# Kernel optimization log

Measured on AMD Instinct MI355X. Metric: run time of the kernel, lower is better.

Reference implementation:

```python
import jax, jax.numpy as jnp
import numpy as np

AGENT_RADIUS = 0.5
SAFETY_DIST = 0.1
QP_ITERS = 300


def _qp_solve(p, G, h):
    """Batched QP: min_u 0.5 u^T u + p^T u  s.t.  G u <= h  (Q = I).
    Solved in the dual by projected gradient ascent (differentiable, fixed iters).
    p: [B,2], G: [B,m,2], h: [B,m] -> u: [B,2]
    """
    GGt = jnp.einsum('bmi,bni->bmn', G, G)                 # [B,m,m]
    q = jnp.einsum('bmi,bi->bm', G, p) + h                 # [B,m]
    # Lipschitz upper bound per sample (Frobenius norm of GG^T)
    L = jnp.sqrt(jnp.sum(GGt * GGt, axis=(1, 2))) + 1e-6   # [B]
    alpha = (1.0 / L)[:, None]

    def step(lam, _):
        grad = jnp.einsum('bmn,bn->bm', GGt, lam) + q
        lam = jnp.maximum(lam - alpha * grad, 0.0)
        return lam, None

    lam0 = jnp.zeros_like(h)
    lam, _ = jax.lax.scan(step, lam0, None, length=QP_ITERS)
    u = -p - jnp.einsum('bmi,bm->bi', G, lam)
    return u


def setup_inputs() -> dict:
    key = jax.random.key(0)
    ks = jax.random.split(key, 20)
    B, F, H1, H2 = 8192, 8, 1024, 512

    def w(k, i, o):
        return (jax.random.normal(k, (i, o), jnp.float32) / np.sqrt(i)).astype(jnp.float32)

    obs_xy = jax.random.uniform(ks[17], (8, 2), jnp.float32, -10.0, 10.0)
    obs_r = jax.random.uniform(ks[18], (8, 1), jnp.float32, 0.3, 0.8)
    return {
        'x': jax.random.normal(ks[0], (B, F), jnp.float32),
        'mean': 0.1 * jax.random.normal(ks[1], (F,), jnp.float32),
        'std': jax.random.uniform(ks[2], (F,), jnp.float32, 0.5, 1.5),
        'W1': w(ks[3], F, H1), 'b1': jnp.zeros((H1,), jnp.float32),
        'W21': w(ks[4], H1, H2), 'b21': jnp.zeros((H2,), jnp.float32),
        'W22': w(ks[5], H1, H2), 'b22': jnp.zeros((H2,), jnp.float32),
        'W23': w(ks[6], H1, H2), 'b23': jnp.zeros((H2,), jnp.float32),
        'W31': w(ks[7], H2, 2), 'b31': jnp.zeros((2,), jnp.float32),
        'W32': w(ks[8], H2, 2), 'b32': jnp.zeros((2,), jnp.float32),
        'W33': w(ks[9], H2, 1), 'b33': jnp.zeros((1,), jnp.float32),
        'obstacles': jnp.concatenate([obs_xy, obs_r], axis=1),  # [8,3] (x,y,r)
        'sgn': 1,
    }


def reference(x, mean, std, W1, b1, W21, b21, W22, b22, W23, b23,
              W31, b31, W32, b32, W33, b33, obstacles, sgn):
    B = x.shape[0]
    x0 = x * std + mean                                   # un-normalized state [B,8]

    h1 = jax.nn.relu(x @ W1 + b1)
    x21 = jax.nn.relu(h1 @ W21 + b21)
    x22 = jax.nn.relu(h1 @ W22 + b22)
    x23 = jax.nn.relu(h1 @ W23 + b23)
    x31 = x21 @ W31 + b31                                 # QP linear term p [B,2]
    x32 = 4.0 * jax.nn.sigmoid(x22 @ W32 + b32)           # CBF gains p1,p2 [B,2]
    x33 = 4.0 * jax.nn.sigmoid(x23 @ W33 + b33)           # liveness gain (unused, smg off)

    px, py, theta, v = x0[:, 0], x0[:, 1], x0[:, 2], x0[:, 3]
    st, ct = jnp.sin(theta)[:, None], jnp.cos(theta)[:, None]
    vb = v[:, None]

    # static obstacles broadcast to batch + opponent as last obstacle -> [B, m]
    ox = jnp.concatenate([jnp.broadcast_to(obstacles[:, 0][None], (B, obstacles.shape[0])), x0[:, 4:5]], axis=1)
    oy = jnp.concatenate([jnp.broadcast_to(obstacles[:, 1][None], (B, obstacles.shape[0])), x0[:, 5:6]], axis=1)
    orad = jnp.concatenate([jnp.broadcast_to(obstacles[:, 2][None], (B, obstacles.shape[0])),
                            jnp.full((B, 1), AGENT_RADIUS, x0.dtype)], axis=1)

    R = AGENT_RADIUS + orad + SAFETY_DIST
    dx = px[:, None] - ox                                  # [B,m]
    dy = py[:, None] - oy

    barrier = dx * dx + dy * dy - R * R
    barrier_dot = 2.0 * dx * vb * ct + 2.0 * dy * vb * st
    Lf2b = (2.0 * v * v)[:, None]
    LgLfbu1 = -2.0 * dx * vb * st + 2.0 * dy * vb * ct
    LgLfbu2 = 2.0 * dx * ct + 2.0 * dy * st
    G = jnp.stack([-LgLfbu1, -LgLfbu2], axis=-1)           # [B,m,2]
    p1, p2 = x32[:, 0:1], x32[:, 1:2]
    h = Lf2b + (p1 + p2) * barrier_dot + p1 * p2 * barrier # [B,m]

    u = _qp_solve(x31, G, h)                               # [B,2]
    return u
```

## Files before the change

### kernel.cpp

```cpp
#include <hip/hip_runtime.h>
#include <cstdint>
#include <cstddef>

typedef unsigned short u16;
typedef u16   u16x8  __attribute__((ext_vector_type(8)));
typedef u16   u16x4  __attribute__((ext_vector_type(4)));
typedef __bf16 bf16x8 __attribute__((ext_vector_type(8)));
typedef float f32x4  __attribute__((ext_vector_type(4)));
typedef float f32x2  __attribute__((ext_vector_type(2)));

__device__ __forceinline__ float bf2f(u16 v) {
  unsigned int u = ((unsigned int)v) << 16;
  return __builtin_bit_cast(float, u);
}
__device__ __forceinline__ u16 f2bf(float f) {
  unsigned int x = __builtin_bit_cast(unsigned int, f);
  x += 0x7fffu + ((x >> 16) & 1u);
  return (u16)(x >> 16);
}

__device__ __forceinline__ void gld_lds16(const u16* g, u16* l) {
  __builtin_amdgcn_global_load_lds(
      (const __attribute__((address_space(1))) unsigned int*)g,
      (__attribute__((address_space(3))) unsigned int*)l, 16, 0, 0);
}

__global__ __launch_bounds__(256) void k_prep(const float* __restrict__ W21,
                                              const float* __restrict__ W22,
                                              u16* __restrict__ Wt,
                                              const float* __restrict__ x,
                                              const float* __restrict__ W1,
                                              const float* __restrict__ b1,
                                              u16* __restrict__ h1,
                                              float* __restrict__ head) {
  __shared__ u16 s[64][65];
  const int b = blockIdx.x;
  if (b < 256) {
    const int mat = b >> 7;
    const int tt  = b & 127;
    const int k0  = (tt >> 3) * 64;
    const int n0  = (tt & 7) * 64;
    const float* W = mat ? W22 : W21;
    const int tx = threadIdx.x & 63;
    const int ty = threadIdx.x >> 6;
#pragma unroll
    for (int i = 0; i < 16; ++i) {
      int r = i * 4 + ty;
      s[r][tx] = f2bf(W[(size_t)(k0 + r) * 512 + n0 + tx]);
    }
    __syncthreads();
    const int nbase = mat * 512 + n0;
#pragma unroll
    for (int i = 0; i < 16; ++i) {
      int r = i * 4 + ty;
      Wt[(size_t)(nbase + r) * 1024 + k0 + tx] = s[tx][r];
    }
  } else {
    const int row0 = (b - 256) * 8;
    if (threadIdx.x < 8)
      *(f32x4*)(head + 4 * (size_t)(row0 + threadIdx.x)) = f32x4{0.f, 0.f, 0.f, 0.f};
    const int c4 = threadIdx.x * 4;
    f32x4 bv = *(const f32x4*)(b1 + c4);
    f32x4 acc[8];
#pragma unroll
    for (int r = 0; r < 8; ++r) acc[r] = bv;
#pragma unroll
    for (int f = 0; f < 8; ++f) {
      f32x4 wv = *(const f32x4*)(W1 + f * 1024 + c4);
#pragma unroll
      for (int r = 0; r < 8; ++r) {
        float xv = x[(size_t)(row0 + r) * 8 + f];
#pragma unroll
        for (int e = 0; e < 4; ++e) acc[r][e] = fmaf(xv, wv[e], acc[r][e]);
      }
    }
#pragma unroll
    for (int r = 0; r < 8; ++r) {
      u16x4 o;
#pragma unroll
      for (int e = 0; e < 4; ++e) o[e] = f2bf(fmaxf(acc[r][e], 0.f));
      *(u16x4*)(h1 + (size_t)(row0 + r) * 1024 + c4) = o;
    }
  }
}

__global__ __launch_bounds__(256) void k_gemm(const u16* __restrict__ A,
                                              const u16* __restrict__ Bt,
                                              const float* __restrict__ b21,
                                              const float* __restrict__ b22,
                                              const float* __restrict__ W31,
                                              const float* __restrict__ W32,
                                              float* __restrict__ head) {
  constexpr int K  = 1024;
  constexpr int BK = 64;
  constexpr int NT = K / BK;
  __shared__ u16 As[2][128 * 64];
  __shared__ u16 Bs[2][128 * 64];

  const int t    = threadIdx.x;
  const int row0 = blockIdx.x * 128;
  const int col0 = blockIdx.y * 128;
  const int w    = t >> 6;
  const int lane = t & 63;
  const int wr   = w >> 1, wc = w & 1;
  const int lrow = lane & 15;
  const int kq   = lane >> 4;

  const u16* gA[4];
  const u16* gB[4];
  int lo[4];
#pragma unroll
  for (int m = 0; m < 4; ++m) {
    const int s  = t + 256 * m;
    const int gc = (s & 7) ^ ((s >> 3) & 7);
    gA[m] = A  + (size_t)(row0 + (s >> 3)) * K + gc * 8;
    gB[m] = Bt + (size_t)(col0 + (s >> 3)) * K + gc * 8;
    lo[m] = s * 8;
  }
  const int po0 = (((0 * 4) + kq) ^ (lrow & 7)) * 8;
  const int po1 = (((1 * 4) + kq) ^ (lrow & 7)) * 8;

  f32x4 acc[4][4];
#pragma unroll
  for (int i = 0; i < 4; ++i)
#pragma unroll
    for (int j = 0; j < 4; ++j) acc[i][j] = f32x4{0.f, 0.f, 0.f, 0.f};

#pragma unroll
  for (int m = 0; m < 4; ++m) {
    gld_lds16(gA[m], As[0] + lo[m]);
    gld_lds16(gB[m], Bs[0] + lo[m]);
  }

  for (int kt = 0; kt < NT; ++kt) {
    const int cur = kt & 1, nxt = cur ^ 1;
    __syncthreads();

    if (kt + 1 < NT) {
      const int ko = (kt + 1) * BK;
#pragma unroll
      for (int m = 0; m < 4; ++m) {
        gld_lds16(gA[m] + ko, As[nxt] + lo[m]);
        gld_lds16(gB[m] + ko, Bs[nxt] + lo[m]);
      }
    }

#pragma unroll
    for (int s32 = 0; s32 < 2; ++s32) {
      const int po = s32 ? po1 : po0;
      bf16x8 af[4], bfr[4];
#pragma unroll
      for (int i = 0; i < 4; ++i)
        af[i] = __builtin_bit_cast(bf16x8,
            *(const u16x8*)(As[cur] + (wr * 64 + i * 16 + lrow) * 64 + po));
#pragma unroll
      for (int j = 0; j < 4; ++j)
        bfr[j] = __builtin_bit_cast(bf16x8,
            *(const u16x8*)(Bs[cur] + (wc * 64 + j * 16 + lrow) * 64 + po));
#pragma unroll
      for (int i = 0; i < 4; ++i)
#pragma unroll
        for (int j = 0; j < 4; ++j)
          acc[i][j] = __builtin_amdgcn_mfma_f32_16x16x32_bf16(af[i], bfr[j], acc[i][j], 0, 0, 0);
    }
  }

  const bool isX21 = (col0 < 512);
  const float* Wh  = isX21 ? W31 : W32;
  const int   hoff = isX21 ? 0 : 2;

  float hx[16], hy[16];
#pragma unroll
  for (int n = 0; n < 16; ++n) { hx[n] = 0.f; hy[n] = 0.f; }
#pragma unroll
  for (int j = 0; j < 4; ++j) {
    int col  = col0 + wc * 64 + j * 16 + lrow;
    int wcol = col & 511;
    f32x2 wv = *(const f32x2*)(Wh + 2 * wcol);
    float bias = isX21 ? b21[col] : b22[wcol];
#pragma unroll
    for (int i = 0; i < 4; ++i)
#pragma unroll
      for (int rr = 0; rr < 4; ++rr) {
        float v = fmaxf(acc[i][j][rr] + bias, 0.f);
        hx[i * 4 + rr] = fmaf(v, wv[0], hx[i * 4 + rr]);
        hy[i * 4 + rr] = fmaf(v, wv[1], hy[i * 4 + rr]);
      }
  }
#pragma unroll
  for (int m = 1; m <= 8; m <<= 1) {
#pragma unroll
    for (int n = 0; n < 16; ++n) {
      hx[n] += __shfl_xor(hx[n], m, 64);
      hy[n] += __shfl_xor(hy[n], m, 64);
    }
  }
  if (lrow == 0) {
#pragma unroll
    for (int i = 0; i < 4; ++i)
#pragma unroll
      for (int rr = 0; rr < 4; ++rr) {
        int row = row0 + wr * 64 + i * 16 + kq * 4 + rr;
        atomicAdd(head + 4 * (size_t)row + hoff,     hx[i * 4 + rr]);
        atomicAdd(head + 4 * (size_t)row + hoff + 1, hy[i * 4 + rr]);
      }
  }
}

__global__ __launch_bounds__(256) void k_qp(const float* __restrict__ x,
                                            const float* __restrict__ mean_,
                                            const float* __restrict__ std_,
                                            const float* __restrict__ head,
                                            const float* __restrict__ b31,
                                            const float* __restrict__ b32,
                                            const float* __restrict__ obstacles,
                                            float* __restrict__ out) {
  const int r = blockIdx.x * 256 + threadIdx.x;
  f32x4 hd = *(const f32x4*)(head + 4 * (size_t)r);
  float p0  = hd[0] + b31[0];
  float p1v = hd[1] + b31[1];
  float pp1 = 4.f / (1.f + expf(-(hd[2] + b32[0])));
  float pp2 = 4.f / (1.f + expf(-(hd[3] + b32[1])));

  const f32x4* xp = (const f32x4*)(x + (size_t)r * 8);
  f32x4 xa = xp[0], xb = xp[1];
  float px = xa[0] * std_[0] + mean_[0];
  float py = xa[1] * std_[1] + mean_[1];
  float th = xa[2] * std_[2] + mean_[2];
  float v  = xa[3] * std_[3] + mean_[3];
  float ax = xb[0] * std_[4] + mean_[4];
  float ay = xb[1] * std_[5] + mean_[5];
  float st = sinf(th), ct = cosf(th);
  float Lf2b = 2.f * v * v;

  float G0[9], G1[9], q[9];
  float s00 = 0.f, s01 = 0.f, s11 = 0.f;
#pragma unroll
  for (int m = 0; m < 9; ++m) {
    float ox, oy, orad;
    if (m < 8) {
      ox = obstacles[m * 3]; oy = obstacles[m * 3 + 1]; orad = obstacles[m * 3 + 2];
    } else { ox = ax; oy = ay; orad = 0.5f; }
    float R  = 0.6f + orad;
    float dx = px - ox, dy = py - oy;
    float bar  = dx * dx + dy * dy - R * R;
    float dct  = dx * ct + dy * st;
    float bdot = 2.f * v * dct;
    float g0 = 2.f * v * (dx * st - dy * ct);
    float g1 = -2.f * dct;
    float h  = Lf2b + (pp1 + pp2) * bdot + pp1 * pp2 * bar;
    G0[m] = g0; G1[m] = g1;
    q[m] = g0 * p0 + g1 * p1v + h;
    s00 += g0 * g0; s01 += g0 * g1; s11 += g1 * g1;
  }
  float L = sqrtf(s00 * s00 + 2.f * s01 * s01 + s11 * s11) + 1e-6f;
  float alpha = 1.f / L;

  float lam[9];
#pragma unroll
  for (int m = 0; m < 9; ++m) lam[m] = 0.f;
  for (int it = 0; it < 300; ++it) {
    float pr0[9], pr1[9];
#pragma unroll
    for (int m = 0; m < 9; ++m) { pr0[m] = G0[m] * lam[m]; pr1[m] = G1[m] * lam[m]; }
    float t0 = (((pr0[0] + pr0[1]) + (pr0[2] + pr0[3])) +
                ((pr0[4] + pr0[5]) + (pr0[6] + pr0[7]))) + pr0[8];
    float t1 = (((pr1[0] + pr1[1]) + (pr1[2] + pr1[3])) +
                ((pr1[4] + pr1[5]) + (pr1[6] + pr1[7]))) + pr1[8];
#pragma unroll
    for (int m = 0; m < 9; ++m) {
      float g = fmaf(G0[m], t0, fmaf(G1[m], t1, q[m]));
      lam[m] = fmaxf(fmaf(-alpha, g, lam[m]), 0.f);
    }
  }
  float u0 = -p0, u1 = -p1v;
#pragma unroll
  for (int m = 0; m < 9; ++m) { u0 = fmaf(-G0[m], lam[m], u0); u1 = fmaf(-G1[m], lam[m], u1); }
  *(f32x2*)(out + 2 * (size_t)r) = f32x2{u0, u1};
}

extern "C" void kernel_launch(void* const* d_in, const int* in_sizes, int n_in,
                              void* d_out, int out_size, void* d_ws, size_t ws_size,
                              hipStream_t stream) {
  const float* x    = (const float*)d_in[0];
  const float* mean_= (const float*)d_in[1];
  const float* std_ = (const float*)d_in[2];
  const float* W1   = (const float*)d_in[3];
  const float* b1   = (const float*)d_in[4];
  const float* W21  = (const float*)d_in[5];
  const float* b21  = (const float*)d_in[6];
  const float* W22  = (const float*)d_in[7];
  const float* b22  = (const float*)d_in[8];
  const float* W31  = (const float*)d_in[11];
  const float* b31  = (const float*)d_in[12];
  const float* W32  = (const float*)d_in[13];
  const float* b32  = (const float*)d_in[14];
  const float* obst = (const float*)d_in[17];
  float* out = (float*)d_out;

  char* ws = (char*)d_ws;
  u16*   Wt   = (u16*)ws;
  u16*   h1   = (u16*)(ws + (size_t)(1 << 21));
  float* head = (float*)(ws + (size_t)(1 << 21) + (size_t)(1 << 24));

  k_prep<<<256 + 1024, 256, 0, stream>>>(W21, W22, Wt, x, W1, b1, h1, head);
  k_gemm<<<dim3(64, 8), 256, 0, stream>>>(h1, Wt, b21, b22, W31, W32, head);
  k_qp  <<<32, 256, 0, stream>>>(x, mean_, std_, head, b31, b32, obst, out);
}
```

Before: 165.9 us.

## Fuse prep, GEMM and QP into one cooperative kernel with grid syncs

Merges the three launches (weight transpose plus layer-1, the bf16 MFMA GEMM with head reduction, and the QP solver) into a single cooperative kernel of 512 blocks, separated by grid-wide syncs. The aim is to remove launch gaps and kernel boundaries. The QP phase now spreads its 8192 rows over 128 blocks, one wave per block, instead of 32 full blocks, and packs the dual variables into float2 vectors so the iteration can use packed FMA. The risks are grid-sync overhead, the requirement that all 512 blocks be co-resident (two per CU), and the QP phase leaving most of the grid idle.

```diff
diff --git a/kernel.cpp b/kernel.cpp
--- a/kernel.cpp
+++ b/kernel.cpp
@@ -1,6 +1,9 @@
 #include <hip/hip_runtime.h>
+#include <hip/hip_cooperative_groups.h>
 #include <cstdint>
 #include <cstddef>
+
+namespace cg = cooperative_groups;
 
 typedef unsigned short u16;
 typedef u16   u16x8  __attribute__((ext_vector_type(8)));
@@ -25,258 +28,291 @@
       (__attribute__((address_space(3))) unsigned int*)l, 16, 0, 0);
 }
 
-__global__ __launch_bounds__(256) void k_prep(const float* __restrict__ W21,
-                                              const float* __restrict__ W22,
-                                              u16* __restrict__ Wt,
-                                              const float* __restrict__ x,
-                                              const float* __restrict__ W1,
-                                              const float* __restrict__ b1,
-                                              u16* __restrict__ h1,
-                                              float* __restrict__ head) {
-  __shared__ u16 s[64][65];
-  const int b = blockIdx.x;
-  if (b < 256) {
-    const int mat = b >> 7;
-    const int tt  = b & 127;
-    const int k0  = (tt >> 3) * 64;
-    const int n0  = (tt & 7) * 64;
-    const float* W = mat ? W22 : W21;
-    const int tx = threadIdx.x & 63;
-    const int ty = threadIdx.x >> 6;
-#pragma unroll
-    for (int i = 0; i < 16; ++i) {
-      int r = i * 4 + ty;
-      s[r][tx] = f2bf(W[(size_t)(k0 + r) * 512 + n0 + tx]);
-    }
-    __syncthreads();
-    const int nbase = mat * 512 + n0;
-#pragma unroll
-    for (int i = 0; i < 16; ++i) {
-      int r = i * 4 + ty;
-      Wt[(size_t)(nbase + r) * 1024 + k0 + tx] = s[tx][r];
-    }
-  } else {
-    const int row0 = (b - 256) * 8;
-    if (threadIdx.x < 8)
-      *(f32x4*)(head + 4 * (size_t)(row0 + threadIdx.x)) = f32x4{0.f, 0.f, 0.f, 0.f};
-    const int c4 = threadIdx.x * 4;
-    f32x4 bv = *(const f32x4*)(b1 + c4);
-    f32x4 acc[8];
-#pragma unroll
-    for (int r = 0; r < 8; ++r) acc[r] = bv;
-#pragma unroll
-    for (int f = 0; f < 8; ++f) {
-      f32x4 wv = *(const f32x4*)(W1 + f * 1024 + c4);
-#pragma unroll
-      for (int r = 0; r < 8; ++r) {
-        float xv = x[(size_t)(row0 + r) * 8 + f];
-#pragma unroll
-        for (int e = 0; e < 4; ++e) acc[r][e] = fmaf(xv, wv[e], acc[r][e]);
-      }
-    }
-#pragma unroll
-    for (int r = 0; r < 8; ++r) {
-      u16x4 o;
-#pragma unroll
-      for (int e = 0; e < 4; ++e) o[e] = f2bf(fmaxf(acc[r][e], 0.f));
-      *(u16x4*)(h1 + (size_t)(row0 + r) * 1024 + c4) = o;
-    }
-  }
-}
-
-__global__ __launch_bounds__(256) void k_gemm(const u16* __restrict__ A,
-                                              const u16* __restrict__ Bt,
-                                              const float* __restrict__ b21,
-                                              const float* __restrict__ b22,
-                                              const float* __restrict__ W31,
-                                              const float* __restrict__ W32,
-                                              float* __restrict__ head) {
-  constexpr int K  = 1024;
-  constexpr int BK = 64;
-  constexpr int NT = K / BK;
+__global__ __launch_bounds__(256, 2) void k_fused(
+    const float* __restrict__ x,   const float* __restrict__ mean_,
+    const float* __restrict__ std_,const float* __restrict__ W1,
+    const float* __restrict__ b1,  const float* __restrict__ W21,
+    const float* __restrict__ b21, const float* __restrict__ W22,
+    const float* __restrict__ b22, const float* __restrict__ W31,
+    const float* __restrict__ b31, const float* __restrict__ W32,
+    const float* __restrict__ b32, const float* __restrict__ obstacles,
+    u16* __restrict__ Wt, u16* __restrict__ h1g, float* __restrict__ head,
+    float* __restrict__ out) {
   __shared__ u16 As[2][128 * 64];
   __shared__ u16 Bs[2][128 * 64];
 
-  const int t    = threadIdx.x;
-  const int row0 = blockIdx.x * 128;
-  const int col0 = blockIdx.y * 128;
-  const int w    = t >> 6;
-  const int lane = t & 63;
-  const int wr   = w >> 1, wc = w & 1;
-  const int lrow = lane & 15;
-  const int kq   = lane >> 4;
-
-  const u16* gA[4];
-  const u16* gB[4];
-  int lo[4];
-#pragma unroll
-  for (int m = 0; m < 4; ++m) {
-    const int s  = t + 256 * m;
-    const int gc = (s & 7) ^ ((s >> 3) & 7);
-    gA[m] = A  + (size_t)(row0 + (s >> 3)) * K + gc * 8;
-    gB[m] = Bt + (size_t)(col0 + (s >> 3)) * K + gc * 8;
-    lo[m] = s * 8;
+  const int id = blockIdx.x;
+  const int t  = threadIdx.x;
+
+  {
+    const int row0t = id * 16;
+    if (t < 16)
+      *(f32x4*)(head + 4 * (size_t)(row0t + t)) = f32x4{0.f, 0.f, 0.f, 0.f};
+
+    if (id < 256) {
+      u16 (*s)[65] = (u16(*)[65]) & As[0][0];
+      const int mat = id >> 7;
+      const int tt  = id & 127;
+      const int k0  = (tt >> 3) * 64;
+      const int n0  = (tt & 7) * 64;
+      const float* W = mat ? W22 : W21;
+      const int tx = t & 63;
+      const int ty = t >> 6;
+#pragma unroll
+      for (int i = 0; i < 16; ++i) {
+        int r = i * 4 + ty;
+        s[r][tx] = f2bf(W[(size_t)(k0 + r) * 512 + n0 + tx]);
+      }
+      __syncthreads();
+      const int nbase = mat * 512 + n0;
+#pragma unroll
+      for (int i = 0; i < 16; ++i) {
+        int r = i * 4 + ty;
+        Wt[(size_t)(nbase + r) * 1024 + k0 + tx] = s[tx][r];
+      }
+    }
+
+    const int c4 = t * 4;
+    f32x4 bv = *(const f32x4*)(b1 + c4);
+    for (int g = 0; g < 2; ++g) {
+      const int row0 = row0t + g * 8;
+      f32x4 acc[8];
+#pragma unroll
+      for (int r = 0; r < 8; ++r) acc[r] = bv;
+#pragma unroll
+      for (int f = 0; f < 8; ++f) {
+        f32x4 wv = *(const f32x4*)(W1 + f * 1024 + c4);
+#pragma unroll
+        for (int r = 0; r < 8; ++r) {
+          float xv = x[(size_t)(row0 + r) * 8 + f];
+#pragma unroll
+          for (int e = 0; e < 4; ++e) acc[r][e] = fmaf(xv, wv[e], acc[r][e]);
+        }
+      }
+#pragma unroll
+      for (int r = 0; r < 8; ++r) {
+        u16x4 o;
+#pragma unroll
+        for (int e = 0; e < 4; ++e) o[e] = f2bf(fmaxf(acc[r][e], 0.f));
+        *(u16x4*)(h1g + (size_t)(row0 + r) * 1024 + c4) = o;
+      }
+    }
   }
-  const int po0 = (((0 * 4) + kq) ^ (lrow & 7)) * 8;
-  const int po1 = (((1 * 4) + kq) ^ (lrow & 7)) * 8;
-
-  f32x4 acc[4][4];
-#pragma unroll
-  for (int i = 0; i < 4; ++i)
-#pragma unroll
-    for (int j = 0; j < 4; ++j) acc[i][j] = f32x4{0.f, 0.f, 0.f, 0.f};
-
-#pragma unroll
-  for (int m = 0; m < 4; ++m) {
-    gld_lds16(gA[m], As[0] + lo[m]);
-    gld_lds16(gB[m], Bs[0] + lo[m]);
+
+  cg::this_grid().sync();
+
+  {
+    constexpr int K  = 1024;
+    constexpr int BK = 64;
+    constexpr int NT = K / BK;
+    const int bx = id & 63, by = id >> 6;
+    const int row0 = bx * 128;
+    const int col0 = by * 128;
+    const int w    = t >> 6;
+    const int lane = t & 63;
+    const int wr   = w >> 1, wc = w & 1;
+    const int lrow = lane & 15;
+    const int kq   = lane >> 4;
+
+    const u16* gA[4];
+    const u16* gB[4];
+    int lo[4];
+#pragma unroll
+    for (int m = 0; m < 4; ++m) {
+      const int s  = t + 256 * m;
+      const int gc = (s & 7) ^ ((s >> 3) & 7);
+      gA[m] = h1g + (size_t)(row0 + (s >> 3)) * K + gc * 8;
+      gB[m] = Wt  + (size_t)(col0 + (s >> 3)) * K + gc * 8;
+      lo[m] = s * 8;
+    }
+    const int po0 = (((0 * 4) + kq) ^ (lrow & 7)) * 8;
+    const int po1 = (((1 * 4) + kq) ^ (lrow & 7)) * 8;
+
+    f32x4 acc[4][4];
+#pragma unroll
+    for (int i = 0; i < 4; ++i)
+#pragma unroll
+      for (int j = 0; j < 4; ++j) acc[i][j] = f32x4{0.f, 0.f, 0.f, 0.f};
+
+#pragma unroll
+    for (int m = 0; m < 4; ++m) {
+      gld_lds16(gA[m], As[0] + lo[m]);
+      gld_lds16(gB[m], Bs[0] + lo[m]);
+    }
+
+    for (int kt = 0; kt < NT; ++kt) {
+      const int cur = kt & 1, nxt = cur ^ 1;
+      __syncthreads();
+
+      if (kt + 1 < NT) {
+        const int ko = (kt + 1) * BK;
+#pragma unroll
+        for (int m = 0; m < 4; ++m) {
+          gld_lds16(gA[m] + ko, As[nxt] + lo[m]);
+          gld_lds16(gB[m] + ko, Bs[nxt] + lo[m]);
+        }
+      }
+
+#pragma unroll
+      for (int s32 = 0; s32 < 2; ++s32) {
+        const int po = s32 ? po1 : po0;
+        bf16x8 af[4], bfr[4];
+#pragma unroll
+        for (int i = 0; i < 4; ++i)
+          af[i] = __builtin_bit_cast(bf16x8,
+              *(const u16x8*)(As[cur] + (wr * 64 + i * 16 + lrow) * 64 + po));
+#pragma unroll
+        for (int j = 0; j < 4; ++j)
+          bfr[j] = __builtin_bit_cast(bf16x8,
+              *(const u16x8*)(Bs[cur] + (wc * 64 + j * 16 + lrow) * 64 + po));
+#pragma unroll
+        for (int i = 0; i < 4; ++i)
+#pragma unroll
+          for (int j = 0; j < 4; ++j)
+            acc[i][j] = __builtin_amdgcn_mfma_f32_16x16x32_bf16(af[i], bfr[j], acc[i][j], 0, 0, 0);
+      }
+    }
+
+    const bool isX21 = (col0 < 512);
+    const float* Wh  = isX21 ? W31 : W32;
+    const int   hoff = isX21 ? 0 : 2;
+
+    float hx[16], hy[16];
+#pragma unroll
+    for (int n = 0; n < 16; ++n) { hx[n] = 0.f; hy[n] = 0.f; }
+#pragma unroll
+    for (int j = 0; j < 4; ++j) {
+      int col  = col0 + wc * 64 + j * 16 + lrow;
+      int wcol = col & 511;
+      f32x2 wv = *(const f32x2*)(Wh + 2 * wcol);
+      float bias = isX21 ? b21[col] : b22[wcol];
+#pragma unroll
+      for (int i = 0; i < 4; ++i)
+#pragma unroll
+        for (int rr = 0; rr < 4; ++rr) {
+          float v = fmaxf(acc[i][j][rr] + bias, 0.f);
+          hx[i * 4 + rr] = fmaf(v, wv[0], hx[i * 4 + rr]);
+          hy[i * 4 + rr] = fmaf(v, wv[1], hy[i * 4 + rr]);
+        }
+    }
+#pragma unroll
+    for (int m = 1; m <= 8; m <<= 1) {
+#pragma unroll
+      for (int n = 0; n < 16; ++n) {
+        hx[n] += __shfl_xor(hx[n], m, 64);
+        hy[n] += __shfl_xor(hy[n], m, 64);
+      }
+    }
+    if (lrow == 0) {
+#pragma unroll
+      for (int i = 0; i < 4; ++i)
+#pragma unroll
+        for (int rr = 0; rr < 4; ++rr) {
+          int row = row0 + wr * 64 + i * 16 + kq * 4 + rr;
+          atomicAdd(head + 4 * (size_t)row + hoff,     hx[i * 4 + rr]);
+          atomicAdd(head + 4 * (size_t)row + hoff + 1, hy[i * 4 + rr]);
+        }
+    }
   }
 
-  for (int kt = 0; kt < NT; ++kt) {
-    const int cur = kt & 1, nxt = cur ^ 1;
-    __syncthreads();
-
-    if (kt + 1 < NT) {
-      const int ko = (kt + 1) * BK;
-#pragma unroll
-      for (int m = 0; m < 4; ++m) {
-        gld_lds16(gA[m] + ko, As[nxt] + lo[m]);
-        gld_lds16(gB[m] + ko, Bs[nxt] + lo[m]);
-      }
-    }
-
-#pragma unroll
-    for (int s32 = 0; s32 < 2; ++s32) {
-      const int po = s32 ? po1 : po0;
-      bf16x8 af[4], bfr[4];
-#pragma unroll
-      for (int i = 0; i < 4; ++i)
-        af[i] = __builtin_bit_cast(bf16x8,
-            *(const u16x8*)(As[cur] + (wr * 64 + i * 16 + lrow) * 64 + po));
-#pragma unroll
-      for (int j = 0; j < 4; ++j)
-        bfr[j] = __builtin_bit_cast(bf16x8,
-            *(const u16x8*)(Bs[cur] + (wc * 64 + j * 16 + lrow) * 64 + po));
-#pragma unroll
-      for (int i = 0; i < 4; ++i)
-#pragma unroll
-        for (int j = 0; j < 4; ++j)
-          acc[i][j] = __builtin_amdgcn_mfma_f32_16x16x32_bf16(af[i], bfr[j], acc[i][j], 0, 0, 0);
-    }
+  cg::this_grid().sync();
+
+  if (id < 128 && (t >> 6) == (id & 3)) {
+    const int r = id * 64 + (t & 63);
+    float hd0 = __hip_atomic_load(head + 4 * (size_t)r + 0, __ATOMIC_RELAXED, __HIP_MEMORY_SCOPE_AGENT);
+    float hd1 = __hip_atomic_load(head + 4 * (size_t)r + 1, __ATOMIC_RELAXED, __HIP_MEMORY_SCOPE_AGENT);
+    float hd2 = __hip_atomic_load(head + 4 * (size_t)r + 2, __ATOMIC_RELAXED, __HIP_MEMORY_SCOPE_AGENT);
+    float hd3 = __hip_atomic_load(head + 4 * (size_t)r + 3, __ATOMIC_RELAXED, __HIP_MEMORY_SCOPE_AGENT);
+    float p0  = hd0 + b31[0];
+    float p1v = hd1 + b31[1];
+    float pp1 = 4.f / (1.f + expf(-(hd2 + b32[0])));
+    float pp2 = 4.f / (1.f + expf(-(hd3 + b32[1])));
+
+    const f32x4* xp = (const f32x4*)(x + (size_t)r * 8);
+    f32x4 xa = xp[0], xb = xp[1];
+    float px = xa[0] * std_[0] + mean_[0];
+    float py = xa[1] * std_[1] + mean_[1];
+    float th = xa[2] * std_[2] + mean_[2];
+    float v  = xa[3] * std_[3] + mean_[3];
+    float ax = xb[0] * std_[4] + mean_[4];
+    float ay = xb[1] * std_[5] + mean_[5];
+    float st = sinf(th), ct = cosf(th);
+    float Lf2b = 2.f * v * v;
+
+    float G0[9], G1[9], q[9];
+    float s00 = 0.f, s01 = 0.f, s11 = 0.f;
+#pragma unroll
+    for (int m = 0; m < 9; ++m) {
+      float ox, oy, orad;
+      if (m < 8) {
+        ox = obstacles[m * 3]; oy = obstacles[m * 3 + 1]; orad = obstacles[m * 3 + 2];
+      } else { ox = ax; oy = ay; orad = 0.5f; }
+      float R  = 0.6f + orad;
+      float dx = px - ox, dy = py - oy;
+      float bar  = dx * dx + dy * dy - R * R;
+      float dct  = dx * ct + dy * st;
+      float bdot = 2.f * v * dct;
+      float g0 = 2.f * v * (dx * st - dy * ct);
+      float g1 = -2.f * dct;
+      float h  = Lf2b + (pp1 + pp2) * bdot + pp1 * pp2 * bar;
+      G0[m] = g0; G1[m] = g1;
+      q[m] = g0 * p0 + g1 * p1v + h;
+      s00 += g0 * g0; s01 += g0 * g1; s11 += g1 * g1;
+    }
+    float L = sqrtf(s00 * s00 + 2.f * s01 * s01 + s11 * s11) + 1e-6f;
+    float alpha = 1.f / L;
+
+    f32x2 G0p[4], G1p[4], qp2[4], lamp[4];
+#pragma unroll
+    for (int j = 0; j < 4; ++j) {
+      G0p[j] = f32x2{G0[j], G0[j + 4]};
+      G1p[j] = f32x2{G1[j], G1[j + 4]};
+      qp2[j] = f32x2{q[j],  q[j + 4]};
+      lamp[j] = f32x2{0.f, 0.f};
+    }
+    float G08 = G0[8], G18 = G1[8], q8 = q[8], lam8 = 0.f;
+    const f32x2 nav = {-alpha, -alpha};
+    const f32x2 z2  = {0.f, 0.f};
+
+    for (int it = 0; it < 300; ++it) {
+      f32x2 pv0[4], pv1[4];
+#pragma unroll
+      for (int j = 0; j < 4; ++j) {
+        pv0[j] = G0p[j] * lamp[j];
+        pv1[j] = G1p[j] * lamp[j];
+      }
+      float pr08 = G08 * lam8, pr18 = G18 * lam8;
+      f32x2 c0 = (pv0[0] + pv0[1]) + (pv0[2] + pv0[3]);
+      f32x2 c1 = (pv1[0] + pv1[1]) + (pv1[2] + pv1[3]);
+      float t0 = (c0.x + c0.y) + pr08;
+      float t1 = (c1.x + c1.y) + pr18;
+      f32x2 t0v = {t0, t0}, t1v = {t1, t1};
+#pragma unroll
+      for (int j = 0; j < 4; ++j) {
+        f32x2 g = __builtin_elementwise_fma(G0p[j], t0v,
+                  __builtin_elementwise_fma(G1p[j], t1v, qp2[j]));
+        lamp[j] = __builtin_elementwise_max(
+                  __builtin_elementwise_fma(nav, g, lamp[j]), z2);
+      }
+      float g8 = fmaf(G08, t0, fmaf(G18, t1, q8));
+      lam8 = fmaxf(fmaf(-alpha, g8, lam8), 0.f);
+    }
+
+    float u0 = -p0, u1 = -p1v;
+#pragma unroll
+    for (int j = 0; j < 4; ++j) {
+      u0 = fmaf(-G0p[j].x, lamp[j].x, u0);
+      u1 = fmaf(-G1p[j].x, lamp[j].x, u1);
+    }
+#pragma unroll
+    for (int j = 0; j < 4; ++j) {
+      u0 = fmaf(-G0p[j].y, lamp[j].y, u0);
+      u1 = fmaf(-G1p[j].y, lamp[j].y, u1);
+    }
+    u0 = fmaf(-G08, lam8, u0);
+    u1 = fmaf(-G18, lam8, u1);
+    *(f32x2*)(out + 2 * (size_t)r) = f32x2{u0, u1};
   }
-
-  const bool isX21 = (col0 < 512);
-  const float* Wh  = isX21 ? W31 : W32;
-  const int   hoff = isX21 ? 0 : 2;
-
-  float hx[16], hy[16];
-#pragma unroll
-  for (int n = 0; n < 16; ++n) { hx[n] = 0.f; hy[n] = 0.f; }
-#pragma unroll
-  for (int j = 0; j < 4; ++j) {
-    int col  = col0 + wc * 64 + j * 16 + lrow;
-    int wcol = col & 511;
-    f32x2 wv = *(const f32x2*)(Wh + 2 * wcol);
-    float bias = isX21 ? b21[col] : b22[wcol];
-#pragma unroll
-    for (int i = 0; i < 4; ++i)
-#pragma unroll
-      for (int rr = 0; rr < 4; ++rr) {
-        float v = fmaxf(acc[i][j][rr] + bias, 0.f);
-        hx[i * 4 + rr] = fmaf(v, wv[0], hx[i * 4 + rr]);
-        hy[i * 4 + rr] = fmaf(v, wv[1], hy[i * 4 + rr]);
-      }
-  }
-#pragma unroll
-  for (int m = 1; m <= 8; m <<= 1) {
-#pragma unroll
-    for (int n = 0; n < 16; ++n) {
-      hx[n] += __shfl_xor(hx[n], m, 64);
-      hy[n] += __shfl_xor(hy[n], m, 64);
-    }
-  }
-  if (lrow == 0) {
-#pragma unroll
-    for (int i = 0; i < 4; ++i)
-#pragma unroll
-      for (int rr = 0; rr < 4; ++rr) {
-        int row = row0 + wr * 64 + i * 16 + kq * 4 + rr;
-        atomicAdd(head + 4 * (size_t)row + hoff,     hx[i * 4 + rr]);
-        atomicAdd(head + 4 * (size_t)row + hoff + 1, hy[i * 4 + rr]);
-      }
-  }
-}
-
-__global__ __launch_bounds__(256) void k_qp(const float* __restrict__ x,
-                                            const float* __restrict__ mean_,
-                                            const float* __restrict__ std_,
-                                            const float* __restrict__ head,
-                                            const float* __restrict__ b31,
-                                            const float* __restrict__ b32,
-                                            const float* __restrict__ obstacles,
-                                            float* __restrict__ out) {
-  const int r = blockIdx.x * 256 + threadIdx.x;
-  f32x4 hd = *(const f32x4*)(head + 4 * (size_t)r);
-  float p0  = hd[0] + b31[0];
-  float p1v = hd[1] + b31[1];
-  float pp1 = 4.f / (1.f + expf(-(hd[2] + b32[0])));
-  float pp2 = 4.f / (1.f + expf(-(hd[3] + b32[1])));
-
-  const f32x4* xp = (const f32x4*)(x + (size_t)r * 8);
-  f32x4 xa = xp[0], xb = xp[1];
-  float px = xa[0] * std_[0] + mean_[0];
-  float py = xa[1] * std_[1] + mean_[1];
-  float th = xa[2] * std_[2] + mean_[2];
-  float v  = xa[3] * std_[3] + mean_[3];
-  float ax = xb[0] * std_[4] + mean_[4];
-  float ay = xb[1] * std_[5] + mean_[5];
-  float st = sinf(th), ct = cosf(th);
-  float Lf2b = 2.f * v * v;
-
-  float G0[9], G1[9], q[9];
-  float s00 = 0.f, s01 = 0.f, s11 = 0.f;
-#pragma unroll
-  for (int m = 0; m < 9; ++m) {
-    float ox, oy, orad;
-    if (m < 8) {
-      ox = obstacles[m * 3]; oy = obstacles[m * 3 + 1]; orad = obstacles[m * 3 + 2];
-    } else { ox = ax; oy = ay; orad = 0.5f; }
-    float R  = 0.6f + orad;
-    float dx = px - ox, dy = py - oy;
-    float bar  = dx * dx + dy * dy - R * R;
-    float dct  = dx * ct + dy * st;
-    float bdot = 2.f * v * dct;
-    float g0 = 2.f * v * (dx * st - dy * ct);
-    float g1 = -2.f * dct;
-    float h  = Lf2b + (pp1 + pp2) * bdot + pp1 * pp2 * bar;
-    G0[m] = g0; G1[m] = g1;
-    q[m] = g0 * p0 + g1 * p1v + h;
-    s00 += g0 * g0; s01 += g0 * g1; s11 += g1 * g1;
-  }
-  float L = sqrtf(s00 * s00 + 2.f * s01 * s01 + s11 * s11) + 1e-6f;
-  float alpha = 1.f / L;
-
-  float lam[9];
-#pragma unroll
-  for (int m = 0; m < 9; ++m) lam[m] = 0.f;
-  for (int it = 0; it < 300; ++it) {
-    float pr0[9], pr1[9];
-#pragma unroll
-    for (int m = 0; m < 9; ++m) { pr0[m] = G0[m] * lam[m]; pr1[m] = G1[m] * lam[m]; }
-    float t0 = (((pr0[0] + pr0[1]) + (pr0[2] + pr0[3])) +
-                ((pr0[4] + pr0[5]) + (pr0[6] + pr0[7]))) + pr0[8];
-    float t1 = (((pr1[0] + pr1[1]) + (pr1[2] + pr1[3])) +
-                ((pr1[4] + pr1[5]) + (pr1[6] + pr1[7]))) + pr1[8];
-#pragma unroll
-    for (int m = 0; m < 9; ++m) {
-      float g = fmaf(G0[m], t0, fmaf(G1[m], t1, q[m]));
-      lam[m] = fmaxf(fmaf(-alpha, g, lam[m]), 0.f);
-    }
-  }
-  float u0 = -p0, u1 = -p1v;
-#pragma unroll
-  for (int m = 0; m < 9; ++m) { u0 = fmaf(-G0[m], lam[m], u0); u1 = fmaf(-G1[m], lam[m], u1); }
-  *(f32x2*)(out + 2 * (size_t)r) = f32x2{u0, u1};
 }
 
 extern "C" void kernel_launch(void* const* d_in, const int* in_sizes, int n_in,
@@ -303,7 +339,8 @@
   u16*   h1   = (u16*)(ws + (size_t)(1 << 21));
   float* head = (float*)(ws + (size_t)(1 << 21) + (size_t)(1 << 24));
 
-  k_prep<<<256 + 1024, 256, 0, stream>>>(W21, W22, Wt, x, W1, b1, h1, head);
-  k_gemm<<<dim3(64, 8), 256, 0, stream>>>(h1, Wt, b21, b22, W31, W32, head);
-  k_qp  <<<32, 256, 0, stream>>>(x, mean_, std_, head, b31, b32, obst, out);
-}
+  void* args[] = {&x, &mean_, &std_, &W1, &b1, &W21, &b21, &W22, &b22,
+                  &W31, &b31, &W32, &b32, &obst, &Wt, &h1, &head, &out};
+  hipLaunchCooperativeKernel(reinterpret_cast<void*>(k_fused),
+                             dim3(512), dim3(256), args, 0, stream);
+}
```

Measured after the change: 310.8 us. +87.3%, slower.
